# Performance work log

Hardware: AMD Instinct MI355X
Metric: run time of the kernel (lower is better)

## Reference

```python
import jax, jax.numpy as jnp
import numpy as np

N = 100_000      # num_nodes
E = 1_600_000    # num_edges (avg degree 16)
D = 64           # embedding_dim
L = 3            # num_layers


def setup_inputs() -> dict:
    key = jax.random.key(0)
    k1, k2 = jax.random.split(key)
    edge_index = jax.random.randint(k1, (2, E), 0, N, dtype=jnp.int64)
    edge_weight = jnp.ones((E,), jnp.float32)
    # nn.init.normal_(std=0.1)
    embedding = 0.1 * jax.random.normal(k2, (N, D), dtype=jnp.float32)
    return {"embedding": embedding, "edge_weight": edge_weight, "edge_index": edge_index}


def reference(embedding, edge_weight, edge_index):
    n = embedding.shape[0]
    self_idx = jnp.arange(n, dtype=edge_index.dtype)
    # add_self_loops: append (i, i) with weight 1 (PyG default fill_value)
    row = jnp.concatenate([edge_index[0], self_idx])  # source j
    col = jnp.concatenate([edge_index[1], self_idx])  # target i
    ew = jnp.concatenate([edge_weight, jnp.ones((n,), embedding.dtype)])
    # degree() counts occurrences of row (unweighted)
    deg = jax.ops.segment_sum(jnp.ones_like(ew), row, num_segments=n)
    deg_inv_sqrt = jnp.where(deg > 0, jax.lax.rsqrt(deg), 0.0)
    norm = deg_inv_sqrt[row] * ew * deg_inv_sqrt[col]  # [E+N]

    x = embedding
    acc = embedding  # running sum of layer-0..L embeddings
    for _ in range(L):
        # gather from source, scale, scatter-add to target (dropout off in eval)
        msg = norm[:, None] * x[row]                       # [E+N, D]
        x = jax.ops.segment_sum(msg, col, num_segments=n)  # [N, D]
        acc = acc + x
    return acc / (L + 1)
```

## Files before the change

### kernel.cpp

```cpp
#include <hip/hip_runtime.h>
#include <stdint.h>

#define DIM 64
#define GB 128
#define GSH 7
#define CH 8192
#define TB1 512
#define BINS2 50000
#define RANGES 2
#define NSLICE 64
#define TBH 1024

__device__ __forceinline__ unsigned bf16rne(float f) {
    unsigned u = __float_as_uint(f);
    return (u + 0x7FFFu + ((u >> 16) & 1u)) >> 16;
}
__device__ __forceinline__ unsigned pack2(float lo, float hi) {
    return bf16rne(lo) | (bf16rne(hi) << 16);
}
#define UNPK(u, lo, hi) { lo = __uint_as_float((u) << 16); hi = __uint_as_float((u) & 0xFFFF0000u); }

__global__ void __launch_bounds__(TBH)
hist_src_kernel(const int* __restrict__ src, unsigned short* __restrict__ partials,
                int E, int N, int Es) {
    __shared__ unsigned h32[BINS2 / 2];
    const int b = blockIdx.x;
    const int r = b / NSLICE, s = b % NSLICE;
    const int base = r * BINS2;
    const int hi = min(base + BINS2, N);
    const int nbw = (hi - base + 1) >> 1;
    for (int j = threadIdx.x; j < nbw; j += TBH) h32[j] = 0;
    __syncthreads();
    const int e0 = s * Es, e1 = min(e0 + Es, E);
#pragma unroll 4
    for (int i = e0 + threadIdx.x; i < e1; i += TBH) {
        unsigned j = (unsigned)(src[i] - base);
        if (j < (unsigned)BINS2) atomicAdd(&h32[j >> 1], 1u << ((j & 1) * 16));
    }
    __syncthreads();
    unsigned* part = (unsigned*)(partials + (size_t)s * N + base);
    for (int j = threadIdx.x; j < nbw; j += TBH) part[j] = h32[j];
}

__global__ void __launch_bounds__(256)
merge_dis_kernel(const unsigned short* __restrict__ partials, float* __restrict__ dis, int N) {
    const int i = blockIdx.x * blockDim.x + threadIdx.x;
    if (i >= N) return;
    int od = 0;
    for (int s = 0; s < NSLICE; ++s) od += partials[(size_t)s * N + i];
    dis[i] = rsqrtf((float)od + 1.0f);
}

__global__ void __launch_bounds__(256)
bucket_cnt_kernel(const int* __restrict__ dst, int* __restrict__ bcnt, int E, int NB) {
    __shared__ int h[1024];
    for (int j = threadIdx.x; j < NB; j += 256) h[j] = 0;
    __syncthreads();
    const int chunk = (E + gridDim.x - 1) / gridDim.x;
    const int e0 = blockIdx.x * chunk, e1 = min(e0 + chunk, E);
    for (int i = e0 + threadIdx.x; i < e1; i += 256)
        atomicAdd(&h[((unsigned)dst[i]) >> GSH], 1);
    __syncthreads();
    for (int j = threadIdx.x; j < NB; j += 256)
        if (h[j]) atomicAdd(&bcnt[j], h[j]);
}

__global__ void scan_buckets(const int* __restrict__ bcnt, int* __restrict__ bucket_base,
                             int* __restrict__ cursor, int* __restrict__ offsets,
                             int NB, int N) {
    __shared__ int buf[1024];
    const int t = threadIdx.x;
    int v = (t < NB) ? bcnt[t] : 0;
    buf[t] = v;
    __syncthreads();
    for (int off = 1; off < 1024; off <<= 1) {
        int add = (t >= off) ? buf[t - off] : 0;
        __syncthreads();
        buf[t] += add;
        __syncthreads();
    }
    if (t < NB) { bucket_base[t] = buf[t] - v; cursor[t] = buf[t] - v; }
    if (t == NB - 1) { bucket_base[NB] = buf[t]; offsets[N] = buf[t]; }
}

__global__ void __launch_bounds__(TB1)
part_kernel(const int* __restrict__ src, const int* __restrict__ dst,
            const float* __restrict__ ew, const float* __restrict__ dis,
            int* __restrict__ cursor, int2* __restrict__ staged, int E, int NB) {
    __shared__ int h[1024];
    const int tid = threadIdx.x;
    const int e0 = blockIdx.x * CH;
    const int e1 = min(e0 + CH, E);
    for (int j = tid; j < NB; j += TB1) h[j] = 0;
    __syncthreads();
    int4 d[4];
    int ngrp = 0;
    for (int i = e0 + tid * 4, k = 0; i < e1; i += TB1 * 4, ++k) {
        int4 t;
        if (i + 3 < e1) t = *(const int4*)(dst + i);
        else {
            t.x = dst[i];
            t.y = (i + 1 < e1) ? dst[i + 1] : -1;
            t.z = (i + 2 < e1) ? dst[i + 2] : -1;
            t.w = (i + 3 < e1) ? dst[i + 3] : -1;
        }
        d[k] = t;
        if (t.x >= 0) atomicAdd(&h[t.x >> GSH], 1);
        if (t.y >= 0) atomicAdd(&h[t.y >> GSH], 1);
        if (t.z >= 0) atomicAdd(&h[t.z >> GSH], 1);
        if (t.w >= 0) atomicAdd(&h[t.w >> GSH], 1);
        ngrp = k + 1;
    }
    __syncthreads();
    for (int j = tid; j < NB; j += TB1) {
        int c = h[j];
        h[j] = c ? atomicAdd(&cursor[j], c) : 0;
    }
    __syncthreads();
    for (int i = e0 + tid * 4, k = 0; k < ngrp; i += TB1 * 4, ++k) {
        int4 t = d[k];
        int4 ss = make_int4(0, 0, 0, 0);
        float4 ww = make_float4(0.f, 0.f, 0.f, 0.f);
        if (i + 3 < e1) { ss = *(const int4*)(src + i); ww = *(const float4*)(ew + i); }
        else {
            ss.x = src[i]; ww.x = ew[i];
            if (i + 1 < e1) { ss.y = src[i + 1]; ww.y = ew[i + 1]; }
            if (i + 2 < e1) { ss.z = src[i + 2]; ww.z = ew[i + 2]; }
            if (i + 3 < e1) { ss.w = src[i + 3]; ww.w = ew[i + 3]; }
        }
#define PART1(T, S, W) if ((T) >= 0) { \
        float w_ = dis[S] * (W) * dis[T]; \
        int pos_ = atomicAdd(&h[(T) >> GSH], 1); \
        staged[pos_] = make_int2((S) | (((T) & (GB - 1)) << 20), __float_as_int(w_)); }
        PART1(t.x, ss.x, ww.x)
        PART1(t.y, ss.y, ww.y)
        PART1(t.z, ss.z, ww.z)
        PART1(t.w, ss.w, ww.w)
#undef PART1
    }
}

__global__ void __launch_bounds__(256)
place_kernel(const int2* __restrict__ staged, const int* __restrict__ bucket_base,
             int* __restrict__ offsets, int2* __restrict__ csr, int N) {
    __shared__ int cnt[GB];
    __shared__ int cur[GB];
    __shared__ int pre[GB + 1];
    const int b = blockIdx.x;
    const int n0 = b << GSH;
    const int nb = min(GB, N - n0);
    const int r0 = bucket_base[b], r1 = bucket_base[b + 1];
    for (int j = threadIdx.x; j < GB; j += 256) cnt[j] = 0;
    __syncthreads();
    for (int i = r0 + threadIdx.x; i < r1; i += 256)
        atomicAdd(&cnt[(staged[i].x >> 20) & (GB - 1)], 1);
    __syncthreads();
    if (threadIdx.x == 0) {
        int run = r0;
        for (int j = 0; j < nb; ++j) { pre[j] = run; run += cnt[j]; }
        pre[nb] = run;
    }
    __syncthreads();
    for (int j = threadIdx.x; j < nb; j += 256) { offsets[n0 + j] = pre[j]; cur[j] = pre[j]; }
    __syncthreads();
    for (int i = r0 + threadIdx.x; i < r1; i += 256) {
        int2 rec = staged[i];
        int tl = (rec.x >> 20) & (GB - 1);
        int rank = atomicAdd(&cur[tl], 1);
        csr[rank] = make_int2(rec.x & 0xFFFFF, rec.y);
    }
}

__global__ void __launch_bounds__(256)
conv_kernel(const float4* __restrict__ in4, uint4* __restrict__ outb, int n8) {
    int i = blockIdx.x * blockDim.x + threadIdx.x;
    if (i >= n8) return;
    float4 a = in4[2 * i], b = in4[2 * i + 1];
    uint4 o;
    o.x = pack2(a.x, a.y); o.y = pack2(a.z, a.w);
    o.z = pack2(b.x, b.y); o.w = pack2(b.z, b.w);
    outb[i] = o;
}

__global__ void __launch_bounds__(256)
prop_kernel(const uint4* __restrict__ xg, const float4* __restrict__ selfF,
            uint4* __restrict__ xstore,
            const int* __restrict__ offsets, const int2* __restrict__ csr,
            const float* __restrict__ dis, int n) {
    const int lane = threadIdx.x & 63;
    const int fl  = lane & 7;
    const int sub = lane >> 3;
    const int wave = blockIdx.x * (blockDim.x >> 6) + (threadIdx.x >> 6);
    const int node = wave * 8 + sub;
    if (node >= n) return;

    const int beg = offsets[node];
    const int end = offsets[node + 1];
    const float d = dis[node];
    const float dd = d * d;

    float a0, a1, a2, a3, a4, a5, a6, a7;
    if (selfF) {
        float4 s0 = selfF[node * 16 + fl * 2];
        float4 s1 = selfF[node * 16 + fl * 2 + 1];
        a0 = dd * s0.x; a1 = dd * s0.y; a2 = dd * s0.z; a3 = dd * s0.w;
        a4 = dd * s1.x; a5 = dd * s1.y; a6 = dd * s1.z; a7 = dd * s1.w;
    } else {
        uint4 q = xg[(size_t)node * 8 + fl];
        float l, h;
        UNPK(q.x, l, h) a0 = dd * l; a1 = dd * h;
        UNPK(q.y, l, h) a2 = dd * l; a3 = dd * h;
        UNPK(q.z, l, h) a4 = dd * l; a5 = dd * h;
        UNPK(q.w, l, h) a6 = dd * l; a7 = dd * h;
    }

#define EDGE(E, Q) { float w_ = __int_as_float((E).y); float l, h; \
    UNPK((Q).x, l, h) a0 = fmaf(w_, l, a0); a1 = fmaf(w_, h, a1); \
    UNPK((Q).y, l, h) a2 = fmaf(w_, l, a2); a3 = fmaf(w_, h, a3); \
    UNPK((Q).z, l, h) a4 = fmaf(w_, l, a4); a5 = fmaf(w_, h, a5); \
    UNPK((Q).w, l, h) a6 = fmaf(w_, l, a6); a7 = fmaf(w_, h, a7); }

    int p = beg;
    for (; p + 8 <= end; p += 8) {
        int2 e0 = csr[p + 0], e1 = csr[p + 1], e2 = csr[p + 2], e3 = csr[p + 3];
        int2 e4 = csr[p + 4], e5 = csr[p + 5], e6 = csr[p + 6], e7 = csr[p + 7];
        uint4 q0 = xg[(size_t)e0.x * 8 + fl];
        uint4 q1 = xg[(size_t)e1.x * 8 + fl];
        uint4 q2 = xg[(size_t)e2.x * 8 + fl];
        uint4 q3 = xg[(size_t)e3.x * 8 + fl];
        uint4 q4 = xg[(size_t)e4.x * 8 + fl];
        uint4 q5 = xg[(size_t)e5.x * 8 + fl];
        uint4 q6 = xg[(size_t)e6.x * 8 + fl];
        uint4 q7 = xg[(size_t)e7.x * 8 + fl];
        EDGE(e0, q0) EDGE(e1, q1) EDGE(e2, q2) EDGE(e3, q3)
        EDGE(e4, q4) EDGE(e5, q5) EDGE(e6, q6) EDGE(e7, q7)
    }
    for (; p + 4 <= end; p += 4) {
        int2 e0 = csr[p + 0], e1 = csr[p + 1], e2 = csr[p + 2], e3 = csr[p + 3];
        uint4 q0 = xg[(size_t)e0.x * 8 + fl];
        uint4 q1 = xg[(size_t)e1.x * 8 + fl];
        uint4 q2 = xg[(size_t)e2.x * 8 + fl];
        uint4 q3 = xg[(size_t)e3.x * 8 + fl];
        EDGE(e0, q0) EDGE(e1, q1) EDGE(e2, q2) EDGE(e3, q3)
    }
    for (; p < end; ++p) {
        int2 e = csr[p];
        uint4 q = xg[(size_t)e.x * 8 + fl];
        EDGE(e, q)
    }
#undef EDGE

    uint4 o;
    o.x = pack2(a0, a1); o.y = pack2(a2, a3);
    o.z = pack2(a4, a5); o.w = pack2(a6, a7);
    xstore[(size_t)node * 8 + fl] = o;
}

__global__ void __launch_bounds__(256)
combine_kernel(const float4* __restrict__ emb4, const uint4* __restrict__ xa,
               const uint4* __restrict__ xb, const uint4* __restrict__ xc,
               float4* __restrict__ out4, int n8) {
    int i = blockIdx.x * blockDim.x + threadIdx.x;
    if (i >= n8) return;
    float4 e0 = emb4[2 * i], e1 = emb4[2 * i + 1];
    uint4 qa = xa[i], qb = xb[i], qc = xc[i];
    float r[8] = { e0.x, e0.y, e0.z, e0.w, e1.x, e1.y, e1.z, e1.w };
    float l, h;
    UNPK(qa.x, l, h) r[0] += l; r[1] += h;
    UNPK(qa.y, l, h) r[2] += l; r[3] += h;
    UNPK(qa.z, l, h) r[4] += l; r[5] += h;
    UNPK(qa.w, l, h) r[6] += l; r[7] += h;
    UNPK(qb.x, l, h) r[0] += l; r[1] += h;
    UNPK(qb.y, l, h) r[2] += l; r[3] += h;
    UNPK(qb.z, l, h) r[4] += l; r[5] += h;
    UNPK(qb.w, l, h) r[6] += l; r[7] += h;
    UNPK(qc.x, l, h) r[0] += l; r[1] += h;
    UNPK(qc.y, l, h) r[2] += l; r[3] += h;
    UNPK(qc.z, l, h) r[4] += l; r[5] += h;
    UNPK(qc.w, l, h) r[6] += l; r[7] += h;
    out4[2 * i]     = make_float4(0.25f * r[0], 0.25f * r[1], 0.25f * r[2], 0.25f * r[3]);
    out4[2 * i + 1] = make_float4(0.25f * r[4], 0.25f * r[5], 0.25f * r[6], 0.25f * r[7]);
}


extern "C" void kernel_launch(void* const* d_in, const int* in_sizes, int n_in,
                              void* d_out, int out_size, void* d_ws, size_t ws_size,
                              hipStream_t stream) {
    const float* emb = (const float*)d_in[0];
    const float* ew  = (const float*)d_in[1];
    const int*   ei  = (const int*)d_in[2];
    const int E = in_sizes[2] / 2;
    const int N = in_sizes[0] / DIM;
    const int* src = ei;
    const int* dst = ei + E;
    float* out = (float*)d_out;

    const int NB = (N + GB - 1) >> GSH;
    const int Es = (E + NSLICE - 1) / NSLICE;

    char* w = (char*)d_ws;
    size_t xSz = ((size_t)N * DIM * 2 + 255) & ~(size_t)255;
    size_t sSz = ((size_t)E * 8 + 255) & ~(size_t)255;
    size_t pSz = ((size_t)NSLICE * N * 2 + 255) & ~(size_t)255;
    size_t uSz = xSz > sSz ? xSz : sSz; if (pSz > uSz) uSz = pSz;
    unsigned short* partials = (unsigned short*)w;
    int2* staged = (int2*)w;
    uint4* xb    = (uint4*)w; w += uSz;
    int2* csr    = (int2*)w; w += sSz;
    uint4* x0c   = (uint4*)w; w += xSz;
    uint4* xa    = (uint4*)w; w += xSz;
    uint4* xc    = (uint4*)w; w += xSz;
    int* offsets = (int*)w; w += ((size_t)(N + 1) * 4 + 255) & ~(size_t)255;
    float* dis   = (float*)w; w += ((size_t)N * 4 + 255) & ~(size_t)255;
    int* bcnt        = (int*)w; w += 1024 * 4;
    int* bucket_base = (int*)w; w += 1025 * 4;
    int* cursor      = (int*)w; w += 1024 * 4;

    const int TB = 256;
    hipMemsetAsync(bcnt, 0, (size_t)NB * 4, stream);

    hist_src_kernel<<<RANGES * NSLICE, TBH, 0, stream>>>(src, partials, E, N, Es);
    bucket_cnt_kernel<<<256, TB, 0, stream>>>(dst, bcnt, E, NB);
    merge_dis_kernel<<<(N + TB - 1) / TB, TB, 0, stream>>>(partials, dis, N);
    scan_buckets<<<1, 1024, 0, stream>>>(bcnt, bucket_base, cursor, offsets, NB, N);
    part_kernel<<<(E + CH - 1) / CH, TB1, 0, stream>>>(src, dst, ew, dis, cursor,
                                                       staged, E, NB);
    place_kernel<<<NB, TB, 0, stream>>>(staged, bucket_base, offsets, csr, N);

    const int n8 = N * DIM / 8;
    conv_kernel<<<(n8 + TB - 1) / TB, TB, 0, stream>>>((const float4*)emb, x0c, n8);

    dim3 grid((N + 31) / 32), block(TB);
    prop_kernel<<<grid, block, 0, stream>>>(x0c, (const float4*)emb, xa,
                                            offsets, csr, dis, N);
    prop_kernel<<<grid, block, 0, stream>>>(xa, nullptr, xb,
                                            offsets, csr, dis, N);
    prop_kernel<<<grid, block, 0, stream>>>(xb, nullptr, xc,
                                            offsets, csr, dis, N);
    combine_kernel<<<(n8 + TB - 1) / TB, TB, 0, stream>>>((const float4*)emb, xa, xb, xc,
                                                          (float4*)out, n8);
}
```

Measured before the change: 284.6 us.

## Fuse bucket count into histogram, stage partition writes in LDS, fuse combine into last prop

```diff
diff --git a/kernel.cpp b/kernel.cpp
--- a/kernel.cpp
+++ b/kernel.cpp
@@ -21,25 +21,40 @@
 #define UNPK(u, lo, hi) { lo = __uint_as_float((u) << 16); hi = __uint_as_float((u) & 0xFFFF0000u); }
 
 __global__ void __launch_bounds__(TBH)
-hist_src_kernel(const int* __restrict__ src, unsigned short* __restrict__ partials,
-                int E, int N, int Es) {
+hist_src_kernel(const int* __restrict__ src, const int* __restrict__ dst,
+                unsigned short* __restrict__ partials, int* __restrict__ bcnt,
+                int E, int N, int Es, int NB) {
     __shared__ unsigned h32[BINS2 / 2];
+    __shared__ int hb[1024];
     const int b = blockIdx.x;
     const int r = b / NSLICE, s = b % NSLICE;
     const int base = r * BINS2;
     const int hi = min(base + BINS2, N);
     const int nbw = (hi - base + 1) >> 1;
     for (int j = threadIdx.x; j < nbw; j += TBH) h32[j] = 0;
+    if (r == 0) for (int j = threadIdx.x; j < NB; j += TBH) hb[j] = 0;
     __syncthreads();
     const int e0 = s * Es, e1 = min(e0 + Es, E);
+    if (r == 0) {
 #pragma unroll 4
-    for (int i = e0 + threadIdx.x; i < e1; i += TBH) {
-        unsigned j = (unsigned)(src[i] - base);
-        if (j < (unsigned)BINS2) atomicAdd(&h32[j >> 1], 1u << ((j & 1) * 16));
+        for (int i = e0 + threadIdx.x; i < e1; i += TBH) {
+            unsigned j = (unsigned)(src[i] - base);
+            if (j < (unsigned)BINS2) atomicAdd(&h32[j >> 1], 1u << ((j & 1) * 16));
+            atomicAdd(&hb[((unsigned)dst[i]) >> GSH], 1);
+        }
+    } else {
+#pragma unroll 4
+        for (int i = e0 + threadIdx.x; i < e1; i += TBH) {
+            unsigned j = (unsigned)(src[i] - base);
+            if (j < (unsigned)BINS2) atomicAdd(&h32[j >> 1], 1u << ((j & 1) * 16));
+        }
     }
     __syncthreads();
     unsigned* part = (unsigned*)(partials + (size_t)s * N + base);
     for (int j = threadIdx.x; j < nbw; j += TBH) part[j] = h32[j];
+    if (r == 0)
+        for (int j = threadIdx.x; j < NB; j += TBH)
+            if (hb[j]) atomicAdd(&bcnt[j], hb[j]);
 }
 
 __global__ void __launch_bounds__(256)
@@ -51,20 +66,6 @@
     dis[i] = rsqrtf((float)od + 1.0f);
 }
 
-__global__ void __launch_bounds__(256)
-bucket_cnt_kernel(const int* __restrict__ dst, int* __restrict__ bcnt, int E, int NB) {
-    __shared__ int h[1024];
-    for (int j = threadIdx.x; j < NB; j += 256) h[j] = 0;
-    __syncthreads();
-    const int chunk = (E + gridDim.x - 1) / gridDim.x;
-    const int e0 = blockIdx.x * chunk, e1 = min(e0 + chunk, E);
-    for (int i = e0 + threadIdx.x; i < e1; i += 256)
-        atomicAdd(&h[((unsigned)dst[i]) >> GSH], 1);
-    __syncthreads();
-    for (int j = threadIdx.x; j < NB; j += 256)
-        if (h[j]) atomicAdd(&bcnt[j], h[j]);
-}
-
 __global__ void scan_buckets(const int* __restrict__ bcnt, int* __restrict__ bucket_base,
                              int* __restrict__ cursor, int* __restrict__ offsets,
                              int NB, int N) {
@@ -87,11 +88,16 @@
 part_kernel(const int* __restrict__ src, const int* __restrict__ dst,
             const float* __restrict__ ew, const float* __restrict__ dis,
             int* __restrict__ cursor, int2* __restrict__ staged, int E, int NB) {
+    __shared__ int2 buf[CH];
+    __shared__ int addr[CH];
     __shared__ int h[1024];
+    __shared__ int sc[1024];
+    __shared__ int gb[1024];
     const int tid = threadIdx.x;
     const int e0 = blockIdx.x * CH;
     const int e1 = min(e0 + CH, E);
-    for (int j = tid; j < NB; j += TB1) h[j] = 0;
+    const int nrec = e1 - e0;
+    for (int j = tid; j < 1024; j += TB1) h[j] = 0;
     __syncthreads();
     int4 d[4];
     int ngrp = 0;
@@ -112,9 +118,21 @@
         ngrp = k + 1;
     }
     __syncthreads();
+    sc[tid] = h[tid]; sc[tid + 512] = h[tid + 512];
+    __syncthreads();
+    for (int off = 1; off < 1024; off <<= 1) {
+        int a0 = (tid >= off) ? sc[tid - off] : 0;
+        int a1 = sc[tid + 512 - off];
+        __syncthreads();
+        sc[tid] += a0; sc[tid + 512] += a1;
+        __syncthreads();
+    }
     for (int j = tid; j < NB; j += TB1) {
         int c = h[j];
-        h[j] = c ? atomicAdd(&cursor[j], c) : 0;
+        int ls = sc[j] - c;
+        gb[j] = c ? atomicAdd(&cursor[j], c) : 0;
+        h[j] = ls;
+        sc[j] = ls;
     }
     __syncthreads();
     for (int i = e0 + tid * 4, k = 0; k < ngrp; i += TB1 * 4, ++k) {
@@ -129,15 +147,20 @@
             if (i + 3 < e1) { ss.w = src[i + 3]; ww.w = ew[i + 3]; }
         }
 #define PART1(T, S, W) if ((T) >= 0) { \
+        int b_ = (T) >> GSH; \
         float w_ = dis[S] * (W) * dis[T]; \
-        int pos_ = atomicAdd(&h[(T) >> GSH], 1); \
-        staged[pos_] = make_int2((S) | (((T) & (GB - 1)) << 20), __float_as_int(w_)); }
+        int lp_ = atomicAdd(&h[b_], 1); \
+        buf[lp_] = make_int2((S) | (((T) & (GB - 1)) << 20), __float_as_int(w_)); \
+        addr[lp_] = gb[b_] + (lp_ - sc[b_]); }
         PART1(t.x, ss.x, ww.x)
         PART1(t.y, ss.y, ww.y)
         PART1(t.z, ss.z, ww.z)
         PART1(t.w, ss.w, ww.w)
 #undef PART1
     }
+    __syncthreads();
+    for (int k = tid; k < nrec; k += TB1)
+        staged[addr[k]] = buf[k];
 }
 
 __global__ void __launch_bounds__(256)
@@ -186,7 +209,9 @@
 prop_kernel(const uint4* __restrict__ xg, const float4* __restrict__ selfF,
             uint4* __restrict__ xstore,
             const int* __restrict__ offsets, const int2* __restrict__ csr,
-            const float* __restrict__ dis, int n) {
+            const float* __restrict__ dis, int n,
+            const float4* __restrict__ embF, const uint4* __restrict__ xaF,
+            float4* __restrict__ outF) {
     const int lane = threadIdx.x & 63;
     const int fl  = lane & 7;
     const int sub = lane >> 3;
@@ -200,18 +225,19 @@
     const float dd = d * d;
 
     float a0, a1, a2, a3, a4, a5, a6, a7;
+    uint4 qs = make_uint4(0, 0, 0, 0);
     if (selfF) {
-        float4 s0 = selfF[node * 16 + fl * 2];
-        float4 s1 = selfF[node * 16 + fl * 2 + 1];
+        float4 s0 = selfF[(size_t)node * 16 + fl * 2];
+        float4 s1 = selfF[(size_t)node * 16 + fl * 2 + 1];
         a0 = dd * s0.x; a1 = dd * s0.y; a2 = dd * s0.z; a3 = dd * s0.w;
         a4 = dd * s1.x; a5 = dd * s1.y; a6 = dd * s1.z; a7 = dd * s1.w;
     } else {
-        uint4 q = xg[(size_t)node * 8 + fl];
+        qs = xg[(size_t)node * 8 + fl];
         float l, h;
-        UNPK(q.x, l, h) a0 = dd * l; a1 = dd * h;
-        UNPK(q.y, l, h) a2 = dd * l; a3 = dd * h;
-        UNPK(q.z, l, h) a4 = dd * l; a5 = dd * h;
-        UNPK(q.w, l, h) a6 = dd * l; a7 = dd * h;
+        UNPK(qs.x, l, h) a0 = dd * l; a1 = dd * h;
+        UNPK(qs.y, l, h) a2 = dd * l; a3 = dd * h;
+        UNPK(qs.z, l, h) a4 = dd * l; a5 = dd * h;
+        UNPK(qs.w, l, h) a6 = dd * l; a7 = dd * h;
     }
 
 #define EDGE(E, Q) { float w_ = __int_as_float((E).y); float l, h; \
@@ -250,36 +276,31 @@
     }
 #undef EDGE
 
-    uint4 o;
-    o.x = pack2(a0, a1); o.y = pack2(a2, a3);
-    o.z = pack2(a4, a5); o.w = pack2(a6, a7);
-    xstore[(size_t)node * 8 + fl] = o;
-}
-
-__global__ void __launch_bounds__(256)
-combine_kernel(const float4* __restrict__ emb4, const uint4* __restrict__ xa,
-               const uint4* __restrict__ xb, const uint4* __restrict__ xc,
-               float4* __restrict__ out4, int n8) {
-    int i = blockIdx.x * blockDim.x + threadIdx.x;
-    if (i >= n8) return;
-    float4 e0 = emb4[2 * i], e1 = emb4[2 * i + 1];
-    uint4 qa = xa[i], qb = xb[i], qc = xc[i];
-    float r[8] = { e0.x, e0.y, e0.z, e0.w, e1.x, e1.y, e1.z, e1.w };
-    float l, h;
-    UNPK(qa.x, l, h) r[0] += l; r[1] += h;
-    UNPK(qa.y, l, h) r[2] += l; r[3] += h;
-    UNPK(qa.z, l, h) r[4] += l; r[5] += h;
-    UNPK(qa.w, l, h) r[6] += l; r[7] += h;
-    UNPK(qb.x, l, h) r[0] += l; r[1] += h;
-    UNPK(qb.y, l, h) r[2] += l; r[3] += h;
-    UNPK(qb.z, l, h) r[4] += l; r[5] += h;
-    UNPK(qb.w, l, h) r[6] += l; r[7] += h;
-    UNPK(qc.x, l, h) r[0] += l; r[1] += h;
-    UNPK(qc.y, l, h) r[2] += l; r[3] += h;
-    UNPK(qc.z, l, h) r[4] += l; r[5] += h;
-    UNPK(qc.w, l, h) r[6] += l; r[7] += h;
-    out4[2 * i]     = make_float4(0.25f * r[0], 0.25f * r[1], 0.25f * r[2], 0.25f * r[3]);
-    out4[2 * i + 1] = make_float4(0.25f * r[4], 0.25f * r[5], 0.25f * r[6], 0.25f * r[7]);
+    if (outF) {
+        float4 eA = embF[(size_t)node * 16 + fl * 2];
+        float4 eB = embF[(size_t)node * 16 + fl * 2 + 1];
+        uint4 qa = xaF[(size_t)node * 8 + fl];
+        float r0 = eA.x + a0, r1 = eA.y + a1, r2 = eA.z + a2, r3 = eA.w + a3;
+        float r4 = eB.x + a4, r5 = eB.y + a5, r6 = eB.z + a6, r7 = eB.w + a7;
+        float l, h;
+        UNPK(qa.x, l, h) r0 += l; r1 += h;
+        UNPK(qa.y, l, h) r2 += l; r3 += h;
+        UNPK(qa.z, l, h) r4 += l; r5 += h;
+        UNPK(qa.w, l, h) r6 += l; r7 += h;
+        UNPK(qs.x, l, h) r0 += l; r1 += h;
+        UNPK(qs.y, l, h) r2 += l; r3 += h;
+        UNPK(qs.z, l, h) r4 += l; r5 += h;
+        UNPK(qs.w, l, h) r6 += l; r7 += h;
+        outF[(size_t)node * 16 + fl * 2] =
+            make_float4(0.25f * r0, 0.25f * r1, 0.25f * r2, 0.25f * r3);
+        outF[(size_t)node * 16 + fl * 2 + 1] =
+            make_float4(0.25f * r4, 0.25f * r5, 0.25f * r6, 0.25f * r7);
+    } else {
+        uint4 o;
+        o.x = pack2(a0, a1); o.y = pack2(a2, a3);
+        o.z = pack2(a4, a5); o.w = pack2(a6, a7);
+        xstore[(size_t)node * 8 + fl] = o;
+    }
 }
 
 
@@ -309,7 +330,6 @@
     int2* csr    = (int2*)w; w += sSz;
     uint4* x0c   = (uint4*)w; w += xSz;
     uint4* xa    = (uint4*)w; w += xSz;
-    uint4* xc    = (uint4*)w; w += xSz;
     int* offsets = (int*)w; w += ((size_t)(N + 1) * 4 + 255) & ~(size_t)255;
     float* dis   = (float*)w; w += ((size_t)N * 4 + 255) & ~(size_t)255;
     int* bcnt        = (int*)w; w += 1024 * 4;
@@ -319,8 +339,8 @@
     const int TB = 256;
     hipMemsetAsync(bcnt, 0, (size_t)NB * 4, stream);
 
-    hist_src_kernel<<<RANGES * NSLICE, TBH, 0, stream>>>(src, partials, E, N, Es);
-    bucket_cnt_kernel<<<256, TB, 0, stream>>>(dst, bcnt, E, NB);
+    hist_src_kernel<<<RANGES * NSLICE, TBH, 0, stream>>>(src, dst, partials, bcnt,
+                                                         E, N, Es, NB);
     merge_dis_kernel<<<(N + TB - 1) / TB, TB, 0, stream>>>(partials, dis, N);
     scan_buckets<<<1, 1024, 0, stream>>>(bcnt, bucket_base, cursor, offsets, NB, N);
     part_kernel<<<(E + CH - 1) / CH, TB1, 0, stream>>>(src, dst, ew, dis, cursor,
@@ -332,11 +352,12 @@
 
     dim3 grid((N + 31) / 32), block(TB);
     prop_kernel<<<grid, block, 0, stream>>>(x0c, (const float4*)emb, xa,
-                                            offsets, csr, dis, N);
+                                            offsets, csr, dis, N,
+                                            nullptr, nullptr, nullptr);
     prop_kernel<<<grid, block, 0, stream>>>(xa, nullptr, xb,
-                                            offsets, csr, dis, N);
-    prop_kernel<<<grid, block, 0, stream>>>(xb, nullptr, xc,
-                                            offsets, csr, dis, N);
-    combine_kernel<<<(n8 + TB - 1) / TB, TB, 0, stream>>>((const float4*)emb, xa, xb, xc,
-                                                          (float4*)out, n8);
-}
+                                            offsets, csr, dis, N,
+                                            nullptr, nullptr, nullptr);
+    prop_kernel<<<grid, block, 0, stream>>>(xb, nullptr, nullptr,
+                                            offsets, csr, dis, N,
+                                            (const float4*)emb, xa, (float4*)out);
+}
```

After: 282.1 us. No clear change (-0.9%).
